# Kernel optimization log

Measured on AMD Instinct MI355X. Metric: run time of the kernel, lower is better.

The kernel has to match this reference:

```python
import jax, jax.numpy as jnp
import numpy as np

T, B, D = 2048, 2, 768
H = 8
HD = D // H
FFN = 3072
EPS = 1e-5


def layer_norm(x, g, b):
    mu = jnp.mean(x, axis=-1, keepdims=True)
    var = jnp.mean(jnp.square(x - mu), axis=-1, keepdims=True)
    return (x - mu) * jax.lax.rsqrt(var + EPS) * g + b


def setup_inputs() -> dict:
    key = jax.random.key(0)
    ks = jax.random.split(key, 12)
    s_d = 1.0 / np.sqrt(D)
    s_f = 1.0 / np.sqrt(FFN)
    return {
        "x": jax.random.normal(ks[0], (T, B, D), dtype=jnp.float32),
        "wq": jax.random.uniform(ks[1], (D, D), jnp.float32, -s_d, s_d),
        "bq": jnp.zeros((D,), jnp.float32),
        "wk": jax.random.uniform(ks[2], (D, D), jnp.float32, -s_d, s_d),
        "bk": jnp.zeros((D,), jnp.float32),
        "wv": jax.random.uniform(ks[3], (D, D), jnp.float32, -s_d, s_d),
        "bv": jnp.zeros((D,), jnp.float32),
        "wo": jax.random.uniform(ks[4], (D, D), jnp.float32, -s_d, s_d),
        "bo": jnp.zeros((D,), jnp.float32),
        "ln1_g": jnp.ones((D,), jnp.float32),
        "ln1_b": jnp.zeros((D,), jnp.float32),
        "w1": jax.random.uniform(ks[5], (FFN, D), jnp.float32, -s_d, s_d),
        "b1": jnp.zeros((FFN,), jnp.float32),
        "w2": jax.random.uniform(ks[6], (D, FFN), jnp.float32, -s_f, s_f),
        "b2": jnp.zeros((D,), jnp.float32),
        "ln2_g": jnp.ones((D,), jnp.float32),
        "ln2_b": jnp.zeros((D,), jnp.float32),
    }


def reference(x, wq, bq, wk, bk, wv, bv, wo, bo, ln1_g, ln1_b, w1, b1, w2, b2, ln2_g, ln2_b):
    # x: [T, B, D] (fairseq layout). Post-LN (layer_norm_first=False), relu, eval mode.
    residual = x
    q = (x @ wq.T + bq).reshape(T, B, H, HD)
    k = (x @ wk.T + bk).reshape(T, B, H, HD)
    v = (x @ wv.T + bv).reshape(T, B, H, HD)
    scale = 1.0 / np.sqrt(HD)
    scores = jnp.einsum('tbhd,sbhd->bhts', q, k) * scale  # [B,H,T,T]
    probs = jax.nn.softmax(scores, axis=-1)
    attn = jnp.einsum('bhts,sbhd->tbhd', probs, v).reshape(T, B, D)
    attn = attn @ wo.T + bo
    x = layer_norm(residual + attn, ln1_g, ln1_b)
    residual = x
    h = jax.nn.relu(x @ w1.T + b1)
    x = residual + (h @ w2.T + b2)
    x = layer_norm(x, ln2_g, ln2_b)
    return x
```

## Files before the change

kernel.cpp:

```cpp
#include <hip/hip_runtime.h>
#include <hip/hip_bf16.h>
#include <math.h>

constexpr int T_LEN = 2048;
constexpr int B_SZ  = 2;
constexpr int D_DIM = 768;
constexpr int H_NUM = 8;
constexpr int HD    = 96;
constexpr int FFN   = 3072;
constexpr float EPS = 1e-5f;
constexpr int TB    = T_LEN * B_SZ;
constexpr int QKV_LD = 3 * D_DIM;
constexpr int NSPLIT = 4;
constexpr int CHUNK  = T_LEN / NSPLIT;
constexpr float SC_LOG2E = 0.14724444458547f;

typedef __attribute__((ext_vector_type(8)))  short short8;
typedef __attribute__((ext_vector_type(4)))  short short4v;
typedef __attribute__((ext_vector_type(2)))  short short2v;
typedef __attribute__((ext_vector_type(4)))  float f32x4;
typedef __attribute__((ext_vector_type(16))) float f32x16;

__device__ __forceinline__ short f2bf(float f) {
    union { float f; unsigned u; } v; v.f = f;
    return (short)((v.u + 0x7FFFu + ((v.u >> 16) & 1u)) >> 16);
}
__device__ __forceinline__ float bf2f(short s) {
    union { unsigned u; float f; } v;
    v.u = ((unsigned)(unsigned short)s) << 16;
    return v.f;
}
__device__ __forceinline__ unsigned pkbf(float a, float b) {
    union { __hip_bfloat162 h; unsigned u; } v;
    v.h = __float22bfloat162_rn(make_float2(a, b));
    return v.u;
}

__device__ __forceinline__ void async_ld16(const short* g, short* l) {
    __builtin_amdgcn_global_load_lds(
        (const __attribute__((address_space(1))) unsigned int*)g,
        (__attribute__((address_space(3))) unsigned int*)l, 16, 0, 0);
}

struct CvtArgs {
    const float* src[7];
    short*       dst[7];
    float        scl[7];
    int          end4[7];
};

__global__ __launch_bounds__(256)
void cvt_all(CvtArgs a, int total4) {
    const int i = blockIdx.x * 256 + threadIdx.x;
    if (i >= total4) return;
    int s = 0;
    while (i >= a.end4[s]) ++s;
    const int base = s ? a.end4[s - 1] : 0;
    const int j = i - base;
    const float sc = a.scl[s];
    const float4 v = ((const float4*)a.src[s])[j];
    short4v o;
    o[0] = f2bf(v.x * sc); o[1] = f2bf(v.y * sc);
    o[2] = f2bf(v.z * sc); o[3] = f2bf(v.w * sc);
    *(short4v*)(a.dst[s] + (size_t)j * 4) = o;
}

__global__ __launch_bounds__(256)
void concat_bias(const float* __restrict__ bq, const float* __restrict__ bk,
                 const float* __restrict__ bv, float* __restrict__ dst) {
    const int i = blockIdx.x * 256 + threadIdx.x;
    if (i >= QKV_LD) return;
    dst[i] = (i < 768) ? bq[i] * SC_LOG2E : (i < 1536 ? bk[i - 768] : bv[i - 1536]);
}

template <int BM, int BN, int BK, typename OutT, bool RELU>
__global__ __launch_bounds__(256)
void gemm_mfma(const short* __restrict__ A, const short* __restrict__ W,
               const float* __restrict__ bias, OutT* __restrict__ C,
               int M, int N, int K) {
    constexpr int MI = BM / 32;
    constexpr int NI = BN / 32;
    constexpr int KI = BK / 32;
    static_assert(BM * BK == 4096 && BN * BK == 4096, "4 glds/thread/stage");
    constexpr int ROWSTEP = 2048 / BK;
    __shared__ __align__(16) short As[2][4096];
    __shared__ __align__(16) short Bs[2][4096];

    const int tid  = threadIdx.x;
    const int w    = tid >> 6;
    const int lane = tid & 63;
    const int l16  = lane & 15;
    const int q4   = lane >> 4;
    const int row0 = blockIdx.y * BM;
    const int col0 = blockIdx.x * BN;
    const int wm   = (w >> 1) * (BM / 2);
    const int wn   = (w & 1) * (BN / 2);

    const int mA = tid / (BK / 8);
    const int kA = (tid % (BK / 8)) * 8;
    const short* gA0 = A + (size_t)(row0 + mA) * K + kA;
    const short* gA1 = gA0 + (size_t)ROWSTEP * K;
    const short* gB0 = W + (size_t)(col0 + mA) * K + kA;
    const short* gB1 = gB0 + (size_t)ROWSTEP * K;

    f32x4 acc[MI][NI];
#pragma unroll
    for (int mi = 0; mi < MI; ++mi)
#pragma unroll
        for (int ni = 0; ni < NI; ++ni)
#pragma unroll
            for (int r = 0; r < 4; ++r) acc[mi][ni][r] = 0.f;

    auto stage = [&](int buf) {
        async_ld16(gA0, &As[buf][w * 512]);
        async_ld16(gA1, &As[buf][2048 + w * 512]);
        async_ld16(gB0, &Bs[buf][w * 512]);
        async_ld16(gB1, &Bs[buf][2048 + w * 512]);
        gA0 += BK; gA1 += BK; gB0 += BK; gB1 += BK;
    };
    auto compute = [&](int buf) {
#pragma unroll
        for (int ks = 0; ks < KI; ++ks) {
            short8 af[MI], bfr[NI];
#pragma unroll
            for (int mi = 0; mi < MI; ++mi)
                af[mi] = *(const short8*)&As[buf][(wm + mi * 16 + l16) * BK + ks * 32 + q4 * 8];
#pragma unroll
            for (int ni = 0; ni < NI; ++ni)
                bfr[ni] = *(const short8*)&Bs[buf][(wn + ni * 16 + l16) * BK + ks * 32 + q4 * 8];
#pragma unroll
            for (int mi = 0; mi < MI; ++mi)
#pragma unroll
                for (int ni = 0; ni < NI; ++ni)
                    acc[mi][ni] = __builtin_amdgcn_mfma_f32_16x16x32_bf16(
                        af[mi], bfr[ni], acc[mi][ni], 0, 0, 0);
        }
    };

    stage(0);
    const int NT = K / BK;
    for (int t = 0; t < NT; ++t) {
        const int cur = t & 1;
        if (t + 1 < NT) {
            stage(cur ^ 1);
            asm volatile("s_waitcnt vmcnt(4)" ::: "memory");
        } else {
            asm volatile("s_waitcnt vmcnt(0)" ::: "memory");
        }
        __builtin_amdgcn_s_barrier();
        __builtin_amdgcn_sched_barrier(0);
        compute(cur);
        __builtin_amdgcn_s_barrier();
        __builtin_amdgcn_sched_barrier(0);
    }

    float bcol[NI];
#pragma unroll
    for (int ni = 0; ni < NI; ++ni) bcol[ni] = bias[col0 + wn + ni * 16 + l16];
#pragma unroll
    for (int mi = 0; mi < MI; ++mi) {
#pragma unroll
        for (int r = 0; r < 4; ++r) {
            const int row = row0 + wm + mi * 16 + q4 * 4 + r;
#pragma unroll
            for (int ni = 0; ni < NI; ++ni) {
                float v = acc[mi][ni][r] + bcol[ni];
                if (RELU) v = fmaxf(v, 0.f);
                const int col = col0 + wn + ni * 16 + l16;
                if constexpr (sizeof(OutT) == 2)
                    C[(size_t)row * N + col] = (OutT)f2bf(v);
                else
                    C[(size_t)row * N + col] = v;
            }
        }
    }
}

__global__ __launch_bounds__(256)
void attn_mfma(const short* __restrict__ qkv, short* __restrict__ Opart,
               float* __restrict__ lpart) {
    __shared__ short Ks[2][32][56];
    __shared__ short Vt[128][44];
    __shared__ short Pw[4][32][36];

    const int tid  = threadIdx.x;
    const int w    = tid >> 6;
    const int lane = tid & 63;
    const int l31  = lane & 31;
    const int h5   = lane >> 5;
    const int t0   = blockIdx.x * 128;
    const int bh   = blockIdx.y;
    const int split = blockIdx.z;
    const int b    = bh >> 3;
    const int h    = bh & 7;

    for (int i = tid; i < 32 * 44; i += 256) {
        const int rr = i / 44, cc = i % 44;
        Vt[96 + rr][cc] = (rr == 0 && cc < 32) ? (short)0x3F80 : (short)0;
    }

    short8 qf[6];
    {
        const int qrow = t0 + w * 32 + l31;
        const short* qb = qkv + ((size_t)qrow * B_SZ + b) * QKV_LD + h * HD;
#pragma unroll
        for (int ks = 0; ks < 6; ++ks)
            qf[ks] = *(const short8*)&qb[ks * 16 + h5 * 8];
    }

    const int k_row = tid >> 2;
    const int k_q   = tid & 3;
    const short* gK = qkv + ((size_t)(split * CHUNK + k_row) * B_SZ + b) * QKV_LD
                      + D_DIM + h * HD + k_q * 24;
    const int ll = tid - 128;
    const int dg = (ll & 7) * 12;
    const int kg = (ll >> 3) * 2;
    const short* gV = qkv + ((size_t)(split * CHUNK + kg) * B_SZ + b) * QKV_LD
                      + 2 * D_DIM + h * HD + dg;
    const size_t step  = (size_t)32 * B_SZ * QKV_LD;
    const size_t vrow  = (size_t)B_SZ * QKV_LD;

    f32x16 oacc[4];
#pragma unroll
    for (int nt = 0; nt < 4; ++nt)
#pragma unroll
        for (int r = 0; r < 16; ++r) oacc[nt][r] = 0.f;

    short8  kpf[3];
    short4v vpf[2][3];
    if (w < 2) {
#pragma unroll
        for (int j = 0; j < 3; ++j) kpf[j] = *(const short8*)(gK + j * 8);
    } else {
#pragma unroll
        for (int r = 0; r < 2; ++r)
#pragma unroll
            for (int c = 0; c < 3; ++c)
                vpf[r][c] = *(const short4v*)(gV + r * vrow + c * 4);
    }

    for (int it = 0; it < CHUNK / 32; ++it) {
        __syncthreads();
        if (w < 2) {
#pragma unroll
            for (int j = 0; j < 3; ++j)
                *(short8*)&Ks[k_q >> 1][k_row][(k_q & 1) * 24 + j * 8] = kpf[j];
        } else {
#pragma unroll
            for (int d = 0; d < 12; ++d) {
                short2v t;
                t[0] = vpf[0][d >> 2][d & 3];
                t[1] = vpf[1][d >> 2][d & 3];
                *(short2v*)&Vt[dg + d][kg] = t;
            }
        }
        __syncthreads();

        if (it + 1 < CHUNK / 32) {
            const size_t off = (size_t)(it + 1) * step;
            if (w < 2) {
#pragma unroll
                for (int j = 0; j < 3; ++j)
                    kpf[j] = *(const short8*)(gK + off + j * 8);
            } else {
#pragma unroll
                for (int r = 0; r < 2; ++r)
#pragma unroll
                    for (int c = 0; c < 3; ++c)
                        vpf[r][c] = *(const short4v*)(gV + off + r * vrow + c * 4);
            }
        }

        f32x16 sa;
#pragma unroll
        for (int r = 0; r < 16; ++r) sa[r] = 0.f;
#pragma unroll
        for (int ks = 0; ks < 6; ++ks) {
            const int half = ks / 3;
            const int base = ks * 16 - half * 48;
            const short8 kf = *(const short8*)&Ks[half][l31][base + h5 * 8];
            sa = __builtin_amdgcn_mfma_f32_32x32x16_bf16(qf[ks], kf, sa, 0, 0, 0);
        }

        float pvx[16];
#pragma unroll
        for (int r = 0; r < 16; ++r) pvx[r] = __builtin_amdgcn_exp2f(sa[r]);
#pragma unroll
        for (int rp = 0; rp < 8; ++rp) {
            const unsigned u = pkbf(pvx[2 * rp], pvx[2 * rp + 1]);
            const int row = ((2 * rp) & 3) + 8 * ((2 * rp) >> 2) + 4 * h5;
            Pw[w][row][l31]     = (short)(u & 0xFFFFu);
            Pw[w][row + 1][l31] = (short)(u >> 16);
        }

#pragma unroll
        for (int ks2 = 0; ks2 < 2; ++ks2) {
            const short* pp = &Pw[w][l31][ks2 * 16 + h5 * 8];
            const short4v plo = *(const short4v*)pp;
            const short4v phi = *(const short4v*)(pp + 4);
            const short8 pfr = __builtin_shufflevector(plo, phi, 0, 1, 2, 3, 4, 5, 6, 7);
#pragma unroll
            for (int nt = 0; nt < 4; ++nt) {
                const short* vp = &Vt[nt * 32 + l31][ks2 * 16 + h5 * 8];
                const short4v vlo = *(const short4v*)vp;
                const short4v vhi = *(const short4v*)(vp + 4);
                const short8 vf = __builtin_shufflevector(vlo, vhi, 0, 1, 2, 3, 4, 5, 6, 7);
                oacc[nt] = __builtin_amdgcn_mfma_f32_32x32x16_bf16(pfr, vf, oacc[nt], 0, 0, 0);
            }
        }
    }

#pragma unroll
    for (int r = 0; r < 16; ++r) {
        const int row  = (r & 3) + 8 * (r >> 2) + 4 * h5;
        const int t    = t0 + w * 32 + row;
        const int grow = t * B_SZ + b;
        short* op = Opart + ((size_t)split * TB + grow) * D_DIM + h * HD;
#pragma unroll
        for (int nt = 0; nt < 3; ++nt)
            op[nt * 32 + l31] = f2bf(oacc[nt][r]);
        if (l31 == 0)
            lpart[((size_t)split * TB + grow) * H_NUM + h] = oacc[3][r];
    }
}

__global__ __launch_bounds__(256)
void attn_combine(const short* __restrict__ Opart, const float* __restrict__ lpart,
                  short* __restrict__ ctx) {
    const int row = blockIdx.x;
    const int tid = threadIdx.x;
    if (tid >= 192) return;
    const int d = tid * 4;
    const int h = d / 96;
    float o0 = 0.f, o1 = 0.f, o2 = 0.f, o3 = 0.f, l = 0.f;
#pragma unroll
    for (int c = 0; c < NSPLIT; ++c) {
        const short4v v = *(const short4v*)&Opart[((size_t)c * TB + row) * D_DIM + d];
        o0 += bf2f(v[0]); o1 += bf2f(v[1]); o2 += bf2f(v[2]); o3 += bf2f(v[3]);
        l += lpart[((size_t)c * TB + row) * H_NUM + h];
    }
    const float iv = 1.f / l;
    short4v r;
    r[0] = f2bf(o0 * iv); r[1] = f2bf(o1 * iv);
    r[2] = f2bf(o2 * iv); r[3] = f2bf(o3 * iv);
    *(short4v*)&ctx[(size_t)row * D_DIM + d] = r;
}

template <typename XT, typename OT>
__global__ __launch_bounds__(256)
void ln_residual(const XT* __restrict__ xres, const short* __restrict__ y,
                 const float* __restrict__ g, const float* __restrict__ bb,
                 OT* __restrict__ out) {
    const int row = blockIdx.x;
    const int tid = threadIdx.x;
    const XT*    xr = xres + (size_t)row * D_DIM;
    const short* yr = y + (size_t)row * D_DIM;

    float vals[3];
    float s = 0.f, s2 = 0.f;
#pragma unroll
    for (int i = 0; i < 3; ++i) {
        const int d = tid + i * 256;
        float xv;
        if constexpr (sizeof(XT) == 2) xv = bf2f((short)xr[d]);
        else                           xv = (float)xr[d];
        const float t = xv + bf2f(yr[d]);
        vals[i] = t;
        s += t;
        s2 = fmaf(t, t, s2);
    }
#pragma unroll
    for (int off = 32; off > 0; off >>= 1) {
        s  += __shfl_down(s, off);
        s2 += __shfl_down(s2, off);
    }
    __shared__ float red_s[4], red_s2[4];
    const int wid = tid >> 6, lane = tid & 63;
    if (lane == 0) { red_s[wid] = s; red_s2[wid] = s2; }
    __syncthreads();
    __shared__ float sh_mean, sh_rstd;
    if (tid == 0) {
        const float ts  = red_s[0] + red_s[1] + red_s[2] + red_s[3];
        const float ts2 = red_s2[0] + red_s2[1] + red_s2[2] + red_s2[3];
        const float mean = ts * (1.f / D_DIM);
        const float var  = ts2 * (1.f / D_DIM) - mean * mean;
        sh_mean = mean;
        sh_rstd = rsqrtf(var + EPS);
    }
    __syncthreads();
    const float mean = sh_mean, rstd = sh_rstd;
#pragma unroll
    for (int i = 0; i < 3; ++i) {
        const int d = tid + i * 256;
        const float o = (vals[i] - mean) * rstd * g[d] + bb[d];
        if constexpr (sizeof(OT) == 2)
            out[(size_t)row * D_DIM + d] = (OT)f2bf(o);
        else
            out[(size_t)row * D_DIM + d] = o;
    }
}

extern "C" void kernel_launch(void* const* d_in, const int* in_sizes, int n_in,
                              void* d_out, int out_size, void* d_ws, size_t ws_size,
                              hipStream_t stream) {
    const float* x     = (const float*)d_in[0];
    const float* wq    = (const float*)d_in[1];
    const float* bq    = (const float*)d_in[2];
    const float* wk    = (const float*)d_in[3];
    const float* bk    = (const float*)d_in[4];
    const float* wv    = (const float*)d_in[5];
    const float* bv    = (const float*)d_in[6];
    const float* wo    = (const float*)d_in[7];
    const float* bo    = (const float*)d_in[8];
    const float* ln1g  = (const float*)d_in[9];
    const float* ln1b  = (const float*)d_in[10];
    const float* w1    = (const float*)d_in[11];
    const float* b1    = (const float*)d_in[12];
    const float* w2    = (const float*)d_in[13];
    const float* b2    = (const float*)d_in[14];
    const float* ln2g  = (const float*)d_in[15];
    const float* ln2b  = (const float*)d_in[16];
    float* out = (float*)d_out;

    char* ws = (char*)d_ws;
    short* qkvb  = (short*)(ws + 0);
    short* ctxb  = (short*)(ws + 18874368);
    short* hb    = (short*)(ws + 0);
    short* xb    = (short*)(ws + 25165824);
    short* Opart = (short*)(ws + 25165824);
    float* lpart = (float*)(ws + 50331648);
    short* tmpb  = (short*)(ws + 25165824);
    short* x1b   = (short*)(ws + 31457280);
    short* wqkv  = (short*)(ws + 50855936);
    short* wob   = (short*)(ws + 54394880);
    short* w1b   = (short*)(ws + 55574528);
    short* w2b   = (short*)(ws + 60293120);
    float* bqkv  = (float*)(ws + 65011712);

    CvtArgs ca;
    ca.src[0] = x;  ca.dst[0] = xb;   ca.scl[0] = 1.f;
    ca.src[1] = wq; ca.dst[1] = wqkv; ca.scl[1] = SC_LOG2E;
    ca.src[2] = wk; ca.dst[2] = wqkv + 768 * 768;     ca.scl[2] = 1.f;
    ca.src[3] = wv; ca.dst[3] = wqkv + 2 * 768 * 768; ca.scl[3] = 1.f;
    ca.src[4] = wo; ca.dst[4] = wob;  ca.scl[4] = 1.f;
    ca.src[5] = w1; ca.dst[5] = w1b;  ca.scl[5] = 1.f;
    ca.src[6] = w2; ca.dst[6] = w2b;  ca.scl[6] = 1.f;
    const int n4[7] = {TB * D_DIM / 4, 768 * 768 / 4, 768 * 768 / 4, 768 * 768 / 4,
                       768 * 768 / 4, FFN * 768 / 4, 768 * FFN / 4};
    int acc4 = 0;
    for (int i = 0; i < 7; ++i) { acc4 += n4[i]; ca.end4[i] = acc4; }
    cvt_all<<<(acc4 + 255) / 256, 256, 0, stream>>>(ca, acc4);
    concat_bias<<<(QKV_LD + 255) / 256, 256, 0, stream>>>(bq, bk, bv, bqkv);

    gemm_mfma<128, 128, 32, short, false><<<dim3(QKV_LD / 128, TB / 128), 256, 0, stream>>>(
        xb, wqkv, bqkv, qkvb, TB, QKV_LD, D_DIM);

    attn_mfma<<<dim3(T_LEN / 128, B_SZ * H_NUM, NSPLIT), dim3(256), 0, stream>>>(
        qkvb, Opart, lpart);
    attn_combine<<<dim3(TB), 256, 0, stream>>>(Opart, lpart, ctxb);

    gemm_mfma<64, 64, 64, short, false><<<dim3(D_DIM / 64, TB / 64), 256, 0, stream>>>(
        ctxb, wob, bo, tmpb, TB, D_DIM, D_DIM);
    ln_residual<float, short><<<dim3(TB), 256, 0, stream>>>(x, tmpb, ln1g, ln1b, x1b);

    gemm_mfma<128, 128, 32, short, true><<<dim3(FFN / 128, TB / 128), 256, 0, stream>>>(
        x1b, w1b, b1, hb, TB, FFN, D_DIM);
    gemm_mfma<64, 64, 64, short, false><<<dim3(D_DIM / 64, TB / 64), 256, 0, stream>>>(
        hb, w2b, b2, tmpb, TB, D_DIM, FFN);
    ln_residual<short, float><<<dim3(TB), 256, 0, stream>>>(x1b, tmpb, ln2g, ln2b, out);
}
```

Before: 300.0 us.

## Transpose attention MFMAs and pass P via permlane swap instead of LDS

Swaps the MFMA operand order so scores come out transposed, with each lane holding one query row's probabilities. The P fragment for the PV MFMA can then be built in registers with permlane32_swap instead of a round trip through shared memory. The row sum is now accumulated in registers rather than through an extra ones-column MFMA, which drops the fourth output tile and the Pw/Vt padding buffers. It also adds s_setprio around the MFMA blocks and vectorizes the output stores. The risk is subtle lane-mapping errors in the transposed layout.

```diff
diff --git a/kernel.cpp b/kernel.cpp
--- a/kernel.cpp
+++ b/kernel.cpp
@@ -20,6 +20,7 @@
 typedef __attribute__((ext_vector_type(2)))  short short2v;
 typedef __attribute__((ext_vector_type(4)))  float f32x4;
 typedef __attribute__((ext_vector_type(16))) float f32x16;
+typedef __attribute__((ext_vector_type(2)))  int   int2v;
 
 __device__ __forceinline__ short f2bf(float f) {
     union { float f; unsigned u; } v; v.f = f;
@@ -34,6 +35,16 @@
     union { __hip_bfloat162 h; unsigned u; } v;
     v.h = __float22bfloat162_rn(make_float2(a, b));
     return v.u;
+}
+__device__ __forceinline__ short4v pk4(float a, float b, float c, float d) {
+    union { unsigned u[2]; short4v s; } v;
+    v.u[0] = pkbf(a, b); v.u[1] = pkbf(c, d);
+    return v.s;
+}
+__device__ __forceinline__ short8 mk8(int a, int b, int c, int d) {
+    union { int u[4]; short8 s; } v;
+    v.u[0] = a; v.u[1] = b; v.u[2] = c; v.u[3] = d;
+    return v.s;
 }
 
 __device__ __forceinline__ void async_ld16(const short* g, short* l) {
@@ -180,8 +191,7 @@
 void attn_mfma(const short* __restrict__ qkv, short* __restrict__ Opart,
                float* __restrict__ lpart) {
     __shared__ short Ks[2][32][56];
-    __shared__ short Vt[128][44];
-    __shared__ short Pw[4][32][36];
+    __shared__ short Vt[96][44];
 
     const int tid  = threadIdx.x;
     const int w    = tid >> 6;
@@ -193,11 +203,6 @@
     const int split = blockIdx.z;
     const int b    = bh >> 3;
     const int h    = bh & 7;
-
-    for (int i = tid; i < 32 * 44; i += 256) {
-        const int rr = i / 44, cc = i % 44;
-        Vt[96 + rr][cc] = (rr == 0 && cc < 32) ? (short)0x3F80 : (short)0;
-    }
 
     short8 qf[6];
     {
@@ -220,11 +225,12 @@
     const size_t step  = (size_t)32 * B_SZ * QKV_LD;
     const size_t vrow  = (size_t)B_SZ * QKV_LD;
 
-    f32x16 oacc[4];
-#pragma unroll
-    for (int nt = 0; nt < 4; ++nt)
+    f32x16 oacc[3];
+#pragma unroll
+    for (int nt = 0; nt < 3; ++nt)
 #pragma unroll
         for (int r = 0; r < 16; ++r) oacc[nt][r] = 0.f;
+    float dsum = 0.f;
 
     short8  kpf[3];
     short4v vpf[2][3];
@@ -274,54 +280,69 @@
         f32x16 sa;
 #pragma unroll
         for (int r = 0; r < 16; ++r) sa[r] = 0.f;
+        __builtin_amdgcn_s_setprio(1);
 #pragma unroll
         for (int ks = 0; ks < 6; ++ks) {
             const int half = ks / 3;
             const int base = ks * 16 - half * 48;
             const short8 kf = *(const short8*)&Ks[half][l31][base + h5 * 8];
-            sa = __builtin_amdgcn_mfma_f32_32x32x16_bf16(qf[ks], kf, sa, 0, 0, 0);
-        }
+            sa = __builtin_amdgcn_mfma_f32_32x32x16_bf16(kf, qf[ks], sa, 0, 0, 0);
+        }
+        __builtin_amdgcn_s_setprio(0);
 
         float pvx[16];
 #pragma unroll
         for (int r = 0; r < 16; ++r) pvx[r] = __builtin_amdgcn_exp2f(sa[r]);
-#pragma unroll
-        for (int rp = 0; rp < 8; ++rp) {
-            const unsigned u = pkbf(pvx[2 * rp], pvx[2 * rp + 1]);
-            const int row = ((2 * rp) & 3) + 8 * ((2 * rp) >> 2) + 4 * h5;
-            Pw[w][row][l31]     = (short)(u & 0xFFFFu);
-            Pw[w][row + 1][l31] = (short)(u >> 16);
-        }
-
+        dsum += ((pvx[0] + pvx[1]) + (pvx[2] + pvx[3]))
+              + ((pvx[4] + pvx[5]) + (pvx[6] + pvx[7]))
+              + ((pvx[8] + pvx[9]) + (pvx[10] + pvx[11]))
+              + ((pvx[12] + pvx[13]) + (pvx[14] + pvx[15]));
+
+        int wA0 = (int)pkbf(pvx[0],  pvx[1]);
+        int wA1 = (int)pkbf(pvx[2],  pvx[3]);
+        int wA2 = (int)pkbf(pvx[4],  pvx[5]);
+        int wA3 = (int)pkbf(pvx[6],  pvx[7]);
+        int wB0 = (int)pkbf(pvx[8],  pvx[9]);
+        int wB1 = (int)pkbf(pvx[10], pvx[11]);
+        int wB2 = (int)pkbf(pvx[12], pvx[13]);
+        int wB3 = (int)pkbf(pvx[14], pvx[15]);
+        const int2v s0 = __builtin_amdgcn_permlane32_swap(wA0, wA2, false, false);
+        const int2v s1 = __builtin_amdgcn_permlane32_swap(wA1, wA3, false, false);
+        const int2v s2 = __builtin_amdgcn_permlane32_swap(wB0, wB2, false, false);
+        const int2v s3 = __builtin_amdgcn_permlane32_swap(wB1, wB3, false, false);
+        const short8 pf0 = mk8(s0[0], s1[0], s0[1], s1[1]);
+        const short8 pf1 = mk8(s2[0], s3[0], s2[1], s3[1]);
+
+        __builtin_amdgcn_s_setprio(1);
 #pragma unroll
         for (int ks2 = 0; ks2 < 2; ++ks2) {
-            const short* pp = &Pw[w][l31][ks2 * 16 + h5 * 8];
-            const short4v plo = *(const short4v*)pp;
-            const short4v phi = *(const short4v*)(pp + 4);
-            const short8 pfr = __builtin_shufflevector(plo, phi, 0, 1, 2, 3, 4, 5, 6, 7);
-#pragma unroll
-            for (int nt = 0; nt < 4; ++nt) {
+            const short8 pfr = ks2 ? pf1 : pf0;
+#pragma unroll
+            for (int nt = 0; nt < 3; ++nt) {
                 const short* vp = &Vt[nt * 32 + l31][ks2 * 16 + h5 * 8];
                 const short4v vlo = *(const short4v*)vp;
                 const short4v vhi = *(const short4v*)(vp + 4);
                 const short8 vf = __builtin_shufflevector(vlo, vhi, 0, 1, 2, 3, 4, 5, 6, 7);
-                oacc[nt] = __builtin_amdgcn_mfma_f32_32x32x16_bf16(pfr, vf, oacc[nt], 0, 0, 0);
+                oacc[nt] = __builtin_amdgcn_mfma_f32_32x32x16_bf16(vf, pfr, oacc[nt], 0, 0, 0);
             }
         }
-    }
-
-#pragma unroll
-    for (int r = 0; r < 16; ++r) {
-        const int row  = (r & 3) + 8 * (r >> 2) + 4 * h5;
-        const int t    = t0 + w * 32 + row;
-        const int grow = t * B_SZ + b;
-        short* op = Opart + ((size_t)split * TB + grow) * D_DIM + h * HD;
-#pragma unroll
-        for (int nt = 0; nt < 3; ++nt)
-            op[nt * 32 + l31] = f2bf(oacc[nt][r]);
-        if (l31 == 0)
-            lpart[((size_t)split * TB + grow) * H_NUM + h] = oacc[3][r];
-    }
+        __builtin_amdgcn_s_setprio(0);
+    }
+
+    const float other = __shfl_xor(dsum, 32);
+    const float denom = dsum + other;
+    const int qrow = t0 + w * 32 + l31;
+    const int grow = qrow * B_SZ + b;
+    short* op = Opart + ((size_t)split * TB + grow) * D_DIM + h * HD;
+#pragma unroll
+    for (int nt = 0; nt < 3; ++nt)
+#pragma unroll
+        for (int g = 0; g < 4; ++g)
+            *(short4v*)&op[nt * 32 + g * 8 + h5 * 4] =
+                pk4(oacc[nt][4 * g], oacc[nt][4 * g + 1],
+                    oacc[nt][4 * g + 2], oacc[nt][4 * g + 3]);
+    if (lane < 32)
+        lpart[((size_t)split * TB + grow) * H_NUM + h] = denom;
 }
 
 __global__ __launch_bounds__(256)
```

Measured after the change: 299.1 us. About the same (-0.3%).
